# Kernel optimization log

Hardware: AMD Instinct MI355X
Metric: run time of the kernel (lower is better)

The kernel has to match this reference:

```python
import jax, jax.numpy as jnp
import numpy as np

NEG_MIN = float(np.finfo(np.float32).min)
LN_EPS = 1e-05


def _layer_norm(x, g, b):
    m = jnp.mean(x, axis=-1, keepdims=True)
    v = jnp.var(x, axis=-1, keepdims=True)
    return (x - m) * jax.lax.rsqrt(v + LN_EPS) * g + b


def _rel_shift_uni(x):
    # x: [qlen, rlen, bsz, n_head] -- Transformer-XL relative shift
    q, r, b, n = x.shape
    zero_pad = jnp.zeros((q, 1, b, n), x.dtype)
    x_padded = jnp.concatenate([zero_pad, x], axis=1).reshape(r + 1, q, b, n)
    return x_padded[1:].reshape(q, r, b, n)


def setup_inputs() -> dict:
    key = jax.random.key(0)
    ks = jax.random.split(key, 12)
    qlen, bsz, d_model = 2048, 2, 1024
    n_head, d_head, d_inner = 16, 64, 4096

    w = jax.random.normal(ks[0], (qlen, bsz, d_model), dtype=jnp.float32)

    # sinusoidal relative position embedding, positions klen-1 .. 0
    pos_seq = jnp.arange(qlen - 1, -1, -1, dtype=jnp.float32)
    inv_freq = 1.0 / (10000.0 ** (jnp.arange(0, d_model, 2, dtype=jnp.float32) / d_model))
    sinusoid = pos_seq[:, None] * inv_freq[None, :]
    r = jnp.concatenate([jnp.sin(sinusoid), jnp.cos(sinusoid)], axis=-1)  # [qlen, d_model]

    s = 0.02
    r_w_bias = jax.random.normal(ks[1], (n_head, d_head), dtype=jnp.float32) * s
    r_r_bias = jax.random.normal(ks[2], (n_head, d_head), dtype=jnp.float32) * s
    qkv_w = jax.random.normal(ks[3], (d_model, 3 * n_head * d_head), dtype=jnp.float32) * s
    r_net_w = jax.random.normal(ks[4], (d_model, n_head * d_head), dtype=jnp.float32) * s
    o_w = jax.random.normal(ks[5], (n_head * d_head, d_model), dtype=jnp.float32) * s
    ffn_w1 = jax.random.normal(ks[6], (d_model, d_inner), dtype=jnp.float32) * s
    ffn_b1 = jnp.zeros((d_inner,), dtype=jnp.float32)
    ffn_w2 = jax.random.normal(ks[7], (d_inner, d_model), dtype=jnp.float32) * s
    ffn_b2 = jnp.zeros((d_model,), dtype=jnp.float32)
    ln1_g = jnp.ones((d_model,), dtype=jnp.float32)
    ln1_b = jnp.zeros((d_model,), dtype=jnp.float32)
    ln2_g = jnp.ones((d_model,), dtype=jnp.float32)
    ln2_b = jnp.zeros((d_model,), dtype=jnp.float32)

    # causal mask: position j > i is masked (uni-directional attention)
    attn_mask = jnp.triu(jnp.ones((qlen, qlen), dtype=bool), k=1)

    return {"w": w, "r": r, "r_w_bias": r_w_bias, "r_r_bias": r_r_bias,
            "attn_mask": attn_mask, "qkv_w": qkv_w, "r_net_w": r_net_w, "o_w": o_w,
            "ln1_g": ln1_g, "ln1_b": ln1_b, "ffn_w1": ffn_w1, "ffn_b1": ffn_b1,
            "ffn_w2": ffn_w2, "ffn_b2": ffn_b2, "ln2_g": ln2_g, "ln2_b": ln2_b}


def reference(w, r, r_w_bias, r_r_bias, attn_mask, qkv_w, r_net_w, o_w,
              ln1_g, ln1_b, ffn_w1, ffn_b1, ffn_w2, ffn_b2, ln2_g, ln2_b):
    qlen, bsz, d_model = w.shape
    n_head, d_head = r_w_bias.shape
    scale = 1.0 / (d_head ** 0.5)

    # qkv projection (post-lnorm path: no pre-norm)
    w_heads = w @ qkv_w  # [q, b, 3*n*d]
    w_q, w_k, w_v = jnp.split(w_heads, 3, axis=-1)
    w_q = w_q.reshape(qlen, bsz, n_head, d_head)
    w_k = w_k.reshape(qlen, bsz, n_head, d_head)
    w_v = w_v.reshape(qlen, bsz, n_head, d_head)

    r_k = (r @ r_net_w).reshape(r.shape[0], n_head, d_head)  # [rlen, n, d]

    # AC: content term, BD: position term with rel-shift
    AC = jnp.einsum('ibnd,jbnd->ijbn', w_q + r_w_bias, w_k)
    BD = jnp.einsum('ibnd,jnd->ijbn', w_q + r_r_bias, r_k)
    BD = _rel_shift_uni(BD)

    attn_score = (AC + BD) * scale
    attn_score = jnp.where(attn_mask[:, :, None, None], NEG_MIN, attn_score)
    attn_prob = jax.nn.softmax(attn_score, axis=1)  # softmax over key axis j

    attn_vec = jnp.einsum('ijbn,jbnd->ibnd', attn_prob, w_v)
    attn_vec = attn_vec.reshape(qlen, bsz, n_head * d_head)
    attn_out = attn_vec @ o_w

    x = _layer_norm(w + attn_out, ln1_g, ln1_b)  # post-lnorm

    # PositionwiseFF (post-lnorm, eval: dropout inactive)
    core = jax.nn.relu(x @ ffn_w1 + ffn_b1) @ ffn_w2 + ffn_b2
    out = _layer_norm(x + core, ln2_g, ln2_b)
    return out
```

## Files before the change

kernel.cpp:

```cpp
#include <hip/hip_runtime.h>
#include <math.h>


typedef __attribute__((ext_vector_type(8))) short short8;
typedef __attribute__((ext_vector_type(4))) float floatx4;

__device__ inline unsigned short f2bf(float f) {
  union { float f; unsigned u; } v; v.f = f;
  unsigned r = v.u + 0x7FFFu + ((v.u >> 16) & 1u);
  return (unsigned short)(r >> 16);
}
__device__ inline float bf2f(unsigned short u) {
  union { unsigned u; float f; } v; v.u = ((unsigned)u) << 16; return v.f;
}

__global__ __launch_bounds__(256) void prep_kernel(
    const float* __restrict__ w, unsigned short* __restrict__ wb,
    const float* __restrict__ r, unsigned short* __restrict__ rb,
    const float* __restrict__ qkv_w, unsigned short* __restrict__ qkvT,
    const float* __restrict__ r_net_w, unsigned short* __restrict__ rnetT,
    const float* __restrict__ o_w, unsigned short* __restrict__ owT,
    const float* __restrict__ ffn_w1, unsigned short* __restrict__ w1T,
    const float* __restrict__ ffn_w2, unsigned short* __restrict__ w2T) {
  __shared__ __align__(16) unsigned short Ts[64][68];
  const int blk = blockIdx.x;
  const int t = threadIdx.x;
  if (blk < 6144) {
    const float* in = blk < 4096 ? w : r;
    unsigned short* outp = blk < 4096 ? wb : rb;
    const int i = (blk < 4096 ? blk : blk - 4096) * 256 + t;
    float4 v = ((const float4*)in)[i];
    ((ushort4*)outp)[i] =
        make_ushort4(f2bf(v.x), f2bf(v.y), f2bf(v.z), f2bf(v.w));
    return;
  }
  const float* src; unsigned short* dst; int K, N, idx;
  if (blk < 6912)      { src = qkv_w;   dst = qkvT;  K = 1024; N = 3072; idx = blk - 6144; }
  else if (blk < 7168) { src = r_net_w; dst = rnetT; K = 1024; N = 1024; idx = blk - 6912; }
  else if (blk < 7424) { src = o_w;     dst = owT;   K = 1024; N = 1024; idx = blk - 7168; }
  else if (blk < 8448) { src = ffn_w1;  dst = w1T;   K = 1024; N = 4096; idx = blk - 7424; }
  else                 { src = ffn_w2;  dst = w2T;   K = 4096; N = 1024; idx = blk - 8448; }
  const int nbx = N >> 6;
  const int k0 = (idx / nbx) * 64, n0 = (idx % nbx) * 64;
  const int rr = t >> 4, c = (t & 15) * 4;
#pragma unroll
  for (int rb2 = 0; rb2 < 64; rb2 += 16) {
    float4 v = *(const float4*)(src + (size_t)(k0 + rb2 + rr) * N + n0 + c);
    *(ushort4*)&Ts[rb2 + rr][c] =
        make_ushort4(f2bf(v.x), f2bf(v.y), f2bf(v.z), f2bf(v.w));
  }
  __syncthreads();
#pragma unroll
  for (int rb2 = 0; rb2 < 64; rb2 += 16) {
    const int nn = rb2 + rr;
    ushort4 o = make_ushort4(Ts[c + 0][nn], Ts[c + 1][nn],
                             Ts[c + 2][nn], Ts[c + 3][nn]);
    *(ushort4*)(dst + (size_t)(n0 + nn) * K + k0 + c) = o;
  }
}

template<int BIAS, int RELU, int OUT_BF16>
__device__ __forceinline__ void bgemm_body(
    const unsigned short* __restrict__ A, const unsigned short* __restrict__ Bt,
    const float* __restrict__ bias, void* __restrict__ C,
    int M, int N, int Kstride, int Klen, size_t psize,
    int bx, int by, int kz,
    unsigned short* As, unsigned short* Bs) {
  const int t = threadIdx.x;
  const int wv = t >> 6, lane = t & 63, quad = lane >> 4, lq = lane & 15;
  const int m0 = by * 128, n0 = bx * 128;
  const int wvm = (wv >> 1) * 64, wvn = (wv & 1) * 64;

  const int srow = t >> 2;
  const int scol = (t & 3) * 8;
  const size_t koff = (size_t)kz * Klen;
  const unsigned short* Ag = A + (size_t)(m0 + srow) * Kstride + scol + koff;
  const unsigned short* Bg = Bt + (size_t)(n0 + srow) * Kstride + scol + koff;
  unsigned short* AsW0 = As + (size_t)wv * 512;
  unsigned short* AsW1 = As + 4096 + (size_t)wv * 512;
  unsigned short* BsW0 = Bs + (size_t)wv * 512;
  unsigned short* BsW1 = Bs + 4096 + (size_t)wv * 512;

  floatx4 acc[4][4];
#pragma unroll
  for (int am = 0; am < 4; ++am)
#pragma unroll
    for (int bn = 0; bn < 4; ++bn) acc[am][bn] = (floatx4){0.f, 0.f, 0.f, 0.f};

  for (int k0 = 0; k0 < Klen; k0 += 64) {
    __syncthreads();
    __builtin_amdgcn_global_load_lds(
        (const __attribute__((address_space(1))) void*)(Ag + k0),
        (__attribute__((address_space(3))) void*)AsW0, 16, 0, 0);
    __builtin_amdgcn_global_load_lds(
        (const __attribute__((address_space(1))) void*)(Ag + (size_t)64 * Kstride + k0),
        (__attribute__((address_space(3))) void*)(AsW0 + 64 * 32), 16, 0, 0);
    __builtin_amdgcn_global_load_lds(
        (const __attribute__((address_space(1))) void*)(Ag + k0 + 32),
        (__attribute__((address_space(3))) void*)AsW1, 16, 0, 0);
    __builtin_amdgcn_global_load_lds(
        (const __attribute__((address_space(1))) void*)(Ag + (size_t)64 * Kstride + k0 + 32),
        (__attribute__((address_space(3))) void*)(AsW1 + 64 * 32), 16, 0, 0);
    __builtin_amdgcn_global_load_lds(
        (const __attribute__((address_space(1))) void*)(Bg + k0),
        (__attribute__((address_space(3))) void*)BsW0, 16, 0, 0);
    __builtin_amdgcn_global_load_lds(
        (const __attribute__((address_space(1))) void*)(Bg + (size_t)64 * Kstride + k0),
        (__attribute__((address_space(3))) void*)(BsW0 + 64 * 32), 16, 0, 0);
    __builtin_amdgcn_global_load_lds(
        (const __attribute__((address_space(1))) void*)(Bg + k0 + 32),
        (__attribute__((address_space(3))) void*)BsW1, 16, 0, 0);
    __builtin_amdgcn_global_load_lds(
        (const __attribute__((address_space(1))) void*)(Bg + (size_t)64 * Kstride + k0 + 32),
        (__attribute__((address_space(3))) void*)(BsW1 + 64 * 32), 16, 0, 0);
    __syncthreads();

#pragma unroll
    for (int s = 0; s < 2; ++s) {
      const unsigned short* Asub = s ? As + 4096 : As;
      const unsigned short* Bsub = s ? Bs + 4096 : Bs;
      short8 af[4], bf[4];
#pragma unroll
      for (int am = 0; am < 4; ++am)
        af[am] = *(const short8*)&Asub[(wvm + am * 16 + lq) * 32 + quad * 8];
#pragma unroll
      for (int bn = 0; bn < 4; ++bn)
        bf[bn] = *(const short8*)&Bsub[(wvn + bn * 16 + lq) * 32 + quad * 8];
#pragma unroll
      for (int am = 0; am < 4; ++am)
#pragma unroll
        for (int bn = 0; bn < 4; ++bn)
          acc[am][bn] = __builtin_amdgcn_mfma_f32_16x16x32_bf16(
              af[am], bf[bn], acc[am][bn], 0, 0, 0);
    }
  }

  float bs[4] = {0.f, 0.f, 0.f, 0.f};
  if (BIAS) {
    if (kz == 0) {
#pragma unroll
      for (int bn = 0; bn < 4; ++bn) bs[bn] = bias[n0 + wvn + bn * 16 + lq];
    }
  }
  float* Cf = (float*)C + (size_t)kz * psize;
#pragma unroll
  for (int am = 0; am < 4; ++am) {
#pragma unroll
    for (int u = 0; u < 4; ++u) {
      const size_t row = m0 + wvm + am * 16 + quad * 4 + u;
#pragma unroll
      for (int bn = 0; bn < 4; ++bn) {
        const size_t col = n0 + wvn + bn * 16 + lq;
        float v = acc[am][bn][u];
        if (BIAS) v += bs[bn];
        if (RELU) v = fmaxf(v, 0.f);
        if (OUT_BF16) ((unsigned short*)C)[row * N + col] = f2bf(v);
        else          Cf[row * N + col] = v;
      }
    }
  }
}

template<int BIAS, int RELU, int OUT_BF16>
__global__ __launch_bounds__(256) void bgemm_kernel(
    const unsigned short* __restrict__ A, const unsigned short* __restrict__ Bt,
    const float* __restrict__ bias, void* __restrict__ C,
    int M, int N, int Kstride, int Klen, size_t psize) {
  __shared__ __align__(16) unsigned short As[2 * 128 * 32];
  __shared__ __align__(16) unsigned short Bs[2 * 128 * 32];
  bgemm_body<BIAS, RELU, OUT_BF16>(A, Bt, bias, C, M, N, Kstride, Klen, psize,
                                   blockIdx.x, blockIdx.y, blockIdx.z, As, Bs);
}

__global__ __launch_bounds__(256) void qkv_rk_kernel(
    const unsigned short* __restrict__ wb, const unsigned short* __restrict__ qkvT,
    unsigned short* __restrict__ w_heads,
    const unsigned short* __restrict__ rbf, const unsigned short* __restrict__ rnetT,
    unsigned short* __restrict__ rk) {
  __shared__ __align__(16) unsigned short As[2 * 128 * 32];
  __shared__ __align__(16) unsigned short Bs[2 * 128 * 32];
  const int bid = blockIdx.x;
  if (bid < 768) {
    bgemm_body<0, 0, 1>(wb, qkvT, nullptr, w_heads, 4096, 3072, 1024, 1024, 0,
                        bid % 24, bid / 24, 0, As, Bs);
  } else {
    const int b2 = bid - 768;
    bgemm_body<0, 0, 1>(rbf, rnetT, nullptr, rk, 2048, 1024, 1024, 1024, 0,
                        b2 % 8, b2 / 8, 0, As, Bs);
  }
}

__global__ __launch_bounds__(512, 4) void attn_mfma_kernel(
    const unsigned short* __restrict__ w_heads,
    const unsigned short* __restrict__ r_k,
    const float* __restrict__ r_w_bias, const float* __restrict__ r_r_bias,
    unsigned short* __restrict__ attn_vec) {
  __shared__ __align__(16) unsigned short Ks[64 * 72];
  __shared__ __align__(16) unsigned short Vt[64 * 72];
  __shared__ __align__(16) unsigned short Rb[256 * 72];
  __shared__ __align__(16) unsigned short Pl[8 * 16 * 72];

  const int t = threadIdx.x;
  const int wv = t >> 6, lane = t & 63, quad = lane >> 4, lq = lane & 15;
  const int g = blockIdx.x;
  const int qq = g >> 5, bnb = g & 31;
  const int it = (qq < 8) ? (15 - qq) : (qq - 8);
  const int b = bnb & 1, n = bnb >> 1;
  const int i0 = it * 128, iw = i0 + wv * 16;

  const int kr = t >> 3, kc8 = (t & 7) * 8;
  const int vj = t & 31, vc = (t >> 5) * 4;

  short8 qw[2], qr[2];
  {
    const unsigned short* qrow =
        w_heads + (size_t)((iw + lq) * 2 + b) * 3072 + n * 64;
    short8 a0 = *(const short8*)(qrow + quad * 8);
    short8 a1 = *(const short8*)(qrow + 32 + quad * 8);
    const float* wbp = r_w_bias + n * 64;
    const float* rbp = r_r_bias + n * 64;
#pragma unroll
    for (int j = 0; j < 8; ++j) {
      const int k0 = quad * 8 + j, k1 = 32 + quad * 8 + j;
      const float q0 = bf2f((unsigned short)a0[j]);
      const float q1 = bf2f((unsigned short)a1[j]);
      qw[0][j] = (short)f2bf(q0 + wbp[k0]);
      qr[0][j] = (short)f2bf(q0 + rbp[k0]);
      qw[1][j] = (short)f2bf(q1 + wbp[k1]);
      qr[1][j] = (short)f2bf(q1 + rbp[k1]);
    }
  }

  floatx4 o[4];
#pragma unroll
  for (int dt = 0; dt < 4; ++dt) o[dt] = (floatx4){0.f, 0.f, 0.f, 0.f};
  float lrow[4] = {0.f, 0.f, 0.f, 0.f};

  unsigned short* Pw = Pl + wv * (16 * 72);
  const int wb2 = 112 - wv * 16;

  int g_idx[4]; bool g_hi[4];
#pragma unroll
  for (int u = 0; u < 4; ++u) {
    const int s = 15 - (quad * 4 + u);
    g_idx[u] = quad * 16 + ((s + lq) & 15);
    g_hi[u] = (s + lq) >= 16;
  }

  const int pbase0 = 1920 - i0;
  const int jt_end = 2 * it + 2;

#pragma unroll
  for (int bq = 0; bq < 2; ++bq) {
    const int row = pbase0 + bq * 64 + kr;
    const int slot = row & 255;
    *(short8*)&Rb[slot * 72 + kc8] =
        *(const short8*)(r_k + (size_t)row * 1024 + n * 64 + kc8);
  }
  short8 sK, sR;
  ushort4 sVl, sVh;
  {
    const unsigned short* kb =
        w_heads + (size_t)(kr * 2 + b) * 3072 + n * 64 + 1024 + kc8;
    sK = *(const short8*)kb;
    const unsigned short* vbp =
        w_heads + (size_t)((2 * vj) * 2 + b) * 3072 + n * 64 + 2048 + vc;
    sVl = *(const ushort4*)vbp;
    sVh = *(const ushort4*)(vbp + 2 * 3072);
    int pg = pbase0 + 128 + kr; if (pg > 2047) pg = 2047;
    sR = *(const short8*)(r_k + (size_t)pg * 1024 + n * 64 + kc8);
  }

  for (int jt = 0; jt < jt_end; ++jt) {
    const int j0 = jt * 64;
    const int pbase = pbase0 + 64 * jt;
    __syncthreads();

    *(short8*)&Ks[kr * 72 + kc8] = sK;
#pragma unroll
    for (int i2 = 0; i2 < 4; ++i2)
      *(unsigned*)&Vt[(vc + i2) * 72 + 2 * vj] =
          (unsigned)sVl[i2] | ((unsigned)sVh[i2] << 16);
    {
      const int slot = (pbase + 128 + kr) & 255;
      *(short8*)&Rb[slot * 72 + kc8] = sR;
    }

    if (jt + 1 < jt_end) {
      const int j0n = j0 + 64;
      const unsigned short* kb =
          w_heads + (size_t)((j0n + kr) * 2 + b) * 3072 + n * 64 + 1024 + kc8;
      sK = *(const short8*)kb;
      const unsigned short* vbp =
          w_heads + (size_t)((j0n + 2 * vj) * 2 + b) * 3072 + n * 64 + 2048 + vc;
      sVl = *(const ushort4*)vbp;
      sVh = *(const ushort4*)(vbp + 2 * 3072);
      int pg = pbase + 192 + kr; if (pg > 2047) pg = 2047;
      sR = *(const short8*)(r_k + (size_t)pg * 1024 + n * 64 + kc8);
    }
    __syncthreads();

    floatx4 ac[4];
#pragma unroll
    for (int ct = 0; ct < 4; ++ct) {
      short8 b0 = *(const short8*)&Ks[(ct * 16 + lq) * 72 + quad * 8];
      short8 b1 = *(const short8*)&Ks[(ct * 16 + lq) * 72 + 32 + quad * 8];
      floatx4 z = (floatx4){0.f, 0.f, 0.f, 0.f};
      z = __builtin_amdgcn_mfma_f32_16x16x32_bf16(qw[0], b0, z, 0, 0, 0);
      z = __builtin_amdgcn_mfma_f32_16x16x32_bf16(qw[1], b1, z, 0, 0, 0);
      ac[ct] = z;
    }
    floatx4 Tt[5];
#pragma unroll
    for (int pt = 0; pt < 5; ++pt) {
      const int slot = (pbase + wb2 + pt * 16 + lq) & 255;
      short8 b0 = *(const short8*)&Rb[slot * 72 + quad * 8];
      short8 b1 = *(const short8*)&Rb[slot * 72 + 32 + quad * 8];
      floatx4 z = (floatx4){0.f, 0.f, 0.f, 0.f};
      z = __builtin_amdgcn_mfma_f32_16x16x32_bf16(qr[0], b0, z, 0, 0, 0);
      z = __builtin_amdgcn_mfma_f32_16x16x32_bf16(qr[1], b1, z, 0, 0, 0);
      Tt[pt] = z;
    }

#pragma unroll
    for (int u = 0; u < 4; ++u) {
      const int r = quad * 4 + u, i = iw + r;
      float sh[5];
#pragma unroll
      for (int pt = 0; pt < 5; ++pt) sh[pt] = __shfl(Tt[pt][u], g_idx[u]);
#pragma unroll
      for (int ct = 0; ct < 4; ++ct) {
        const float bd = g_hi[u] ? sh[ct + 1] : sh[ct];
        const int j = j0 + ct * 16 + lq;
        const float pr =
            (j <= i) ? __expf((ac[ct][u] + bd) * 0.125f) : 0.f;
        Pw[r * 72 + ct * 16 + lq] = f2bf(pr);
        lrow[u] += pr;
      }
    }

    __builtin_amdgcn_s_waitcnt(0xC07F);

    short8 pA0 = *(const short8*)&Pw[lq * 72 + quad * 8];
    short8 pA1 = *(const short8*)&Pw[lq * 72 + 32 + quad * 8];
#pragma unroll
    for (int dt = 0; dt < 4; ++dt) {
      short8 v0 = *(const short8*)&Vt[(dt * 16 + lq) * 72 + quad * 8];
      short8 v1 = *(const short8*)&Vt[(dt * 16 + lq) * 72 + 32 + quad * 8];
      o[dt] = __builtin_amdgcn_mfma_f32_16x16x32_bf16(pA0, v0, o[dt], 0, 0, 0);
      o[dt] = __builtin_amdgcn_mfma_f32_16x16x32_bf16(pA1, v1, o[dt], 0, 0, 0);
    }
  }

#pragma unroll
  for (int u = 0; u < 4; ++u) {
    float l = lrow[u];
    l += __shfl_xor(l, 1);
    l += __shfl_xor(l, 2);
    l += __shfl_xor(l, 4);
    l += __shfl_xor(l, 8);
    const float linv = 1.f / l;
    const int i = iw + quad * 4 + u;
    unsigned short* op = attn_vec + (size_t)(i * 2 + b) * 1024 + n * 64 + lq;
#pragma unroll
    for (int dt = 0; dt < 4; ++dt) op[dt * 16] = f2bf(o[dt][u] * linv);
  }
}

__global__ __launch_bounds__(256) void ln_res_kernel(
    const float* __restrict__ X, const float* __restrict__ R0,
    const float* __restrict__ R1,
    const float* __restrict__ g, const float* __restrict__ bta,
    float* __restrict__ out, unsigned short* __restrict__ out_bf) {
  const int row = blockIdx.x;
  const int t = threadIdx.x;
  float4 xv = ((const float4*)(X + (size_t)row * 1024))[t];
  float4 rv = ((const float4*)(R0 + (size_t)row * 1024))[t];
  float4 v = make_float4(xv.x + rv.x, xv.y + rv.y, xv.z + rv.z, xv.w + rv.w);
  if (R1) {
    float4 r2 = ((const float4*)(R1 + (size_t)row * 1024))[t];
    v.x += r2.x; v.y += r2.y; v.z += r2.z; v.w += r2.w;
  }
  float s  = v.x + v.y + v.z + v.w;
  float sq = v.x * v.x + v.y * v.y + v.z * v.z + v.w * v.w;
#pragma unroll
  for (int off = 32; off > 0; off >>= 1) {
    s  += __shfl_xor(s, off);
    sq += __shfl_xor(sq, off);
  }
  __shared__ float ss[4], ssq[4];
  const int wid = t >> 6;
  if ((t & 63) == 0) { ss[wid] = s; ssq[wid] = sq; }
  __syncthreads();
  s  = ss[0] + ss[1] + ss[2] + ss[3];
  sq = ssq[0] + ssq[1] + ssq[2] + ssq[3];
  const float mean = s * (1.f / 1024.f);
  const float var  = sq * (1.f / 1024.f) - mean * mean;
  const float inv  = rsqrtf(var + 1e-5f);
  float4 gv = ((const float4*)g)[t];
  float4 bv = ((const float4*)bta)[t];
  float4 ov = make_float4((v.x - mean) * inv * gv.x + bv.x,
                          (v.y - mean) * inv * gv.y + bv.y,
                          (v.z - mean) * inv * gv.z + bv.z,
                          (v.w - mean) * inv * gv.w + bv.w);
  ((float4*)(out + (size_t)row * 1024))[t] = ov;
  if (out_bf)
    ((ushort4*)(out_bf + (size_t)row * 1024))[t] =
        make_ushort4(f2bf(ov.x), f2bf(ov.y), f2bf(ov.z), f2bf(ov.w));
}

extern "C" void kernel_launch(void* const* d_in, const int* in_sizes, int n_in,
                              void* d_out, int out_size, void* d_ws, size_t ws_size,
                              hipStream_t stream) {
  (void)in_sizes; (void)n_in; (void)out_size; (void)ws_size;
  const float* w        = (const float*)d_in[0];
  const float* r        = (const float*)d_in[1];
  const float* r_w_bias = (const float*)d_in[2];
  const float* r_r_bias = (const float*)d_in[3];
  const float* qkv_w    = (const float*)d_in[5];
  const float* r_net_w  = (const float*)d_in[6];
  const float* o_w      = (const float*)d_in[7];
  const float* ln1_g    = (const float*)d_in[8];
  const float* ln1_b    = (const float*)d_in[9];
  const float* ffn_w1   = (const float*)d_in[10];
  const float* ffn_b1   = (const float*)d_in[11];
  const float* ffn_w2   = (const float*)d_in[12];
  const float* ffn_b2   = (const float*)d_in[13];
  const float* ln2_g    = (const float*)d_in[14];
  const float* ln2_b    = (const float*)d_in[15];
  float* out = (float*)d_out;

  char* base = (char*)d_ws;
  const size_t MB = (size_t)1 << 20;
  unsigned short* w_heads = (unsigned short*)(base + 0);
  float*          aout0   = (float*)(base + 0);
  float*          aout1   = (float*)(base + 16 * MB);
  unsigned short* h1      = (unsigned short*)(base + 0);
  float*          x       = (float*)(base + 32 * MB);
  unsigned short* w2T     = (unsigned short*)(base + 48 * MB);
  unsigned short* w1T     = (unsigned short*)(base + 56 * MB);
  float*          core0   = (float*)(base + 56 * MB);
  float*          core1   = (float*)(base + 72 * MB);
  unsigned short* wb      = (unsigned short*)(base + 64 * MB);
  unsigned short* avec    = (unsigned short*)(base + 64 * MB);
  unsigned short* rb      = (unsigned short*)(base + 72 * MB);
  unsigned short* xb      = (unsigned short*)(base + 72 * MB);
  unsigned short* rk      = (unsigned short*)(base + 76 * MB);
  unsigned short* qkvT    = (unsigned short*)(base + 80 * MB);
  unsigned short* owT     = (unsigned short*)(base + 86 * MB);
  unsigned short* rnetT   = (unsigned short*)(base + 88 * MB);

  dim3 blk(256);
  prep_kernel<<<9472, blk, 0, stream>>>(w, wb, r, rb, qkv_w, qkvT,
                                        r_net_w, rnetT, o_w, owT,
                                        ffn_w1, w1T, ffn_w2, w2T);

  qkv_rk_kernel<<<896, blk, 0, stream>>>(wb, qkvT, w_heads, rb, rnetT, rk);
  attn_mfma_kernel<<<512, 512, 0, stream>>>(
      w_heads, rk, r_w_bias, r_r_bias, avec);
  bgemm_kernel<0, 0, 0><<<dim3(8, 32, 2), blk, 0, stream>>>(
      avec, owT, nullptr, aout0, 4096, 1024, 1024, 512, (size_t)4096 * 1024);
  ln_res_kernel<<<4096, blk, 0, stream>>>(w, aout0, aout1, ln1_g, ln1_b, x, xb);
  bgemm_kernel<1, 1, 1><<<dim3(32, 32, 1), blk, 0, stream>>>(
      xb, w1T, ffn_b1, h1, 4096, 4096, 1024, 1024, 0);
  bgemm_kernel<1, 0, 0><<<dim3(8, 32, 2), blk, 0, stream>>>(
      h1, w2T, ffn_b2, core0, 4096, 1024, 4096, 2048, (size_t)4096 * 1024);
  ln_res_kernel<<<4096, blk, 0, stream>>>(x, core0, core1, ln2_g, ln2_b, out, nullptr);
}
```

Before: 423.0 us.

## Streamline attention softmax: raw exp2, packed bf16 convert, swizzled P tile, lighter barriers

Rewrites the per-tile softmax/P-store stage of the attention kernel. It uses v_exp_f32 with a log2e-folded scale instead of __expf, and skips the causal mask check on fully interior tiles. It converts pairs of probabilities with v_cvt_pk_bf16_f32 instead of software rounding, and stores P in an XOR-swizzled layout meant to reduce LDS bank conflicts. __syncthreads is replaced by raw s_barrier with explicit waitcnt to avoid overwaiting on pending global loads. The risks are subtle memory-ordering bugs from the hand-written barriers and differences in bf16 rounding.

```diff
diff --git a/kernel.cpp b/kernel.cpp
--- a/kernel.cpp
+++ b/kernel.cpp
@@ -190,6 +190,8 @@
   }
 }
 
+#define PSWZ(r, cb) ((r) * 144 + ((cb) ^ ((((r) >> 1) & 7) << 4)))
+
 __global__ __launch_bounds__(512, 4) void attn_mfma_kernel(
     const unsigned short* __restrict__ w_heads,
     const unsigned short* __restrict__ r_k,
@@ -274,7 +276,10 @@
   for (int jt = 0; jt < jt_end; ++jt) {
     const int j0 = jt * 64;
     const int pbase = pbase0 + 64 * jt;
-    __syncthreads();
+
+    asm volatile("" ::: "memory");
+    __builtin_amdgcn_s_barrier();
+    asm volatile("" ::: "memory");
 
     *(short8*)&Ks[kr * 72 + kc8] = sK;
 #pragma unroll
@@ -298,7 +303,10 @@
       int pg = pbase + 192 + kr; if (pg > 2047) pg = 2047;
       sR = *(const short8*)(r_k + (size_t)pg * 1024 + n * 64 + kc8);
     }
-    __syncthreads();
+
+    asm volatile("s_waitcnt lgkmcnt(0)" ::: "memory");
+    __builtin_amdgcn_s_barrier();
+    asm volatile("" ::: "memory");
 
     floatx4 ac[4];
 #pragma unroll
@@ -322,27 +330,63 @@
       Tt[pt] = z;
     }
 
-#pragma unroll
-    for (int u = 0; u < 4; ++u) {
-      const int r = quad * 4 + u, i = iw + r;
-      float sh[5];
-#pragma unroll
-      for (int pt = 0; pt < 5; ++pt) sh[pt] = __shfl(Tt[pt][u], g_idx[u]);
+    float p16[4][4];
+    const bool interior = (j0 + 63 <= iw);
+    if (interior) {
+#pragma unroll
+      for (int u = 0; u < 4; ++u) {
+        float sh[5];
+#pragma unroll
+        for (int pt = 0; pt < 5; ++pt) sh[pt] = __shfl(Tt[pt][u], g_idx[u]);
+#pragma unroll
+        for (int ct = 0; ct < 4; ++ct) {
+          const float bd = g_hi[u] ? sh[ct + 1] : sh[ct];
+          const float xs = (ac[ct][u] + bd) * 0.18033688011112042f;
+          float e; asm("v_exp_f32 %0, %1" : "=v"(e) : "v"(xs));
+          p16[u][ct] = e;
+          lrow[u] += e;
+        }
+      }
+    } else {
+#pragma unroll
+      for (int u = 0; u < 4; ++u) {
+        const int i = iw + quad * 4 + u;
+        float sh[5];
+#pragma unroll
+        for (int pt = 0; pt < 5; ++pt) sh[pt] = __shfl(Tt[pt][u], g_idx[u]);
+#pragma unroll
+        for (int ct = 0; ct < 4; ++ct) {
+          const float bd = g_hi[u] ? sh[ct + 1] : sh[ct];
+          const int j = j0 + ct * 16 + lq;
+          const float xs = (ac[ct][u] + bd) * 0.18033688011112042f;
+          float e; asm("v_exp_f32 %0, %1" : "=v"(e) : "v"(xs));
+          e = (j <= i) ? e : 0.f;
+          p16[u][ct] = e;
+          lrow[u] += e;
+        }
+      }
+    }
+
+#pragma unroll
+    for (int up = 0; up < 2; ++up) {
+      const int r0 = quad * 4 + up * 2;
 #pragma unroll
       for (int ct = 0; ct < 4; ++ct) {
-        const float bd = g_hi[u] ? sh[ct + 1] : sh[ct];
-        const int j = j0 + ct * 16 + lq;
-        const float pr =
-            (j <= i) ? __expf((ac[ct][u] + bd) * 0.125f) : 0.f;
-        Pw[r * 72 + ct * 16 + lq] = f2bf(pr);
-        lrow[u] += pr;
+        unsigned pk;
+        asm("v_cvt_pk_bf16_f32 %0, %1, %2"
+            : "=v"(pk)
+            : "v"(p16[up * 2][ct]), "v"(p16[up * 2 + 1][ct]));
+        const int cb = (ct * 16 + lq) * 2;
+        *(unsigned short*)((char*)Pw + PSWZ(r0, cb)) = (unsigned short)pk;
+        *(unsigned short*)((char*)Pw + PSWZ(r0 + 1, cb)) =
+            (unsigned short)(pk >> 16);
       }
     }
 
     __builtin_amdgcn_s_waitcnt(0xC07F);
 
-    short8 pA0 = *(const short8*)&Pw[lq * 72 + quad * 8];
-    short8 pA1 = *(const short8*)&Pw[lq * 72 + 32 + quad * 8];
+    short8 pA0 = *(const short8*)((const char*)Pw + PSWZ(lq, quad * 16));
+    short8 pA1 = *(const short8*)((const char*)Pw + PSWZ(lq, 64 + quad * 16));
 #pragma unroll
     for (int dt = 0; dt < 4; ++dt) {
       short8 v0 = *(const short8*)&Vt[(dt * 16 + lq) * 72 + quad * 8];
```

After: 443.1 us. 1.05x slower.
